# Kernel optimization log

Measured on AMD Instinct MI355X. Metric: run time of the kernel, lower is better.

## Reference

```python
import jax, jax.numpy as jnp
import numpy as np

N_NODES = 1024
BATCH = 64
N = N_NODES * BATCH          # 65536 total nodes
BBX, LBL = 7, 1
H1, H2, H3 = 512, 16, 4096
LAT = 512
NCLS = 160
N_EDGES = 262144


def setup_inputs() -> dict:
    key = jax.random.key(0)
    ks = jax.random.split(key, 20)
    g = lambda k, shape: (jax.random.normal(k, shape, jnp.float32) * 0.02)
    inp = dict(
        E=jax.random.randint(ks[0], (2, N_EDGES), 0, N, dtype=jnp.int64),
        X_data=jax.random.normal(ks[1], (N, BBX + LBL), jnp.float32),
        class_labels=jax.random.uniform(ks[2], (BATCH * NCLS,), jnp.float32),
        # GCNConv weights (no bias, no normalize, no self-loops)
        W_g1=g(ks[3], (BBX + LBL, H1)),
        W_g2=g(ks[4], (H1, H2)),
        # dense layers ([in, out] convention; y = x @ W + b)
        W_box=g(ks[5], (BBX, H2)), b_box=jnp.zeros((H2,), jnp.float32),
        W_lbl=g(ks[6], (LBL, H2)), b_lbl=jnp.zeros((H2,), jnp.float32),
        W_d1=g(ks[7], (H2 * N_NODES, H3)), b_d1=jnp.zeros((H3,), jnp.float32),
        W_d2=g(ks[8], (H2 * N_NODES + NCLS, H3)), b_d2=jnp.zeros((H3,), jnp.float32),
        W_d3=g(ks[9], (H3, H3)), b_d3=jnp.zeros((H3,), jnp.float32),
        W_z=g(ks[10], (H3, LAT)), b_z=jnp.zeros((LAT,), jnp.float32),
    )
    return inp


def reference(E, X_data, class_labels, W_g1, W_g2, W_box, b_box, W_lbl, b_lbl,
              W_d1, b_d1, W_d2, b_d2, W_d3, b_d3, W_z, b_z):
    relu = jax.nn.relu
    src, dst = E[0], E[1]
    # GCNConv (normalize=False, add_self_loops=False, bias=False):
    # out[i] = sum_{(j->i) in E} (x @ W)[j]
    x = jax.ops.segment_sum((X_data @ W_g1)[src], dst, num_segments=N)   # [N, H1]
    x = jax.ops.segment_sum((x @ W_g2)[src], dst, num_segments=N)        # [N, H2]
    x = x.reshape(BATCH, N_NODES * H2)                                   # [B, 16*num_nodes]
    boxes = relu(X_data[:, 1:].reshape(BATCH, N_NODES, BBX) @ W_box + b_box)
    labels = relu(X_data[:, :1].reshape(BATCH, N_NODES, LBL) @ W_lbl + b_lbl)
    mix = (boxes + labels).reshape(BATCH, N_NODES * H2)
    mix = relu(mix @ W_d1 + b_d1)                                        # [B, H3]
    cls = class_labels.reshape(BATCH, NCLS)
    x = jnp.concatenate([cls, x], axis=-1)                               # [B, NCLS + 16*num_nodes]
    x = relu(x @ W_d2 + b_d2)
    x = x + mix
    x = relu(x @ W_d3 + b_d3)
    x = relu(x @ W_d3 + b_d3)
    z_mean = relu(x @ W_z + b_z)
    z_logvar = relu(x @ W_z + b_z)
    return (z_mean, z_logvar)
```

## Files before the change

kernel.cpp:

```cpp
#include <hip/hip_runtime.h>
#include <stdint.h>

typedef unsigned short u16;
typedef short bf16x8 __attribute__((ext_vector_type(8)));
typedef short bf16x4 __attribute__((ext_vector_type(4)));
typedef float f32x4 __attribute__((ext_vector_type(4)));

#define NTOT   65536
#define NB     64
#define NEDGE  262144
#define H3     4096
#define LATD   512
#define NCLS_  160
#define K1     16384
#define K2     16544

static __device__ __forceinline__ u16 f2b(float f) {
  uint32_t x = __float_as_uint(f);
  return (u16)((x + 0x7FFFu + ((x >> 16) & 1u)) >> 16);
}

__global__ void k_hist(const int* __restrict__ E, int* __restrict__ cnt,
                       const float* __restrict__ Wg1, const float* __restrict__ Wg2,
                       float* __restrict__ Wc) {
  int e = blockIdx.x * 256 + threadIdx.x;
  atomicAdd(&cnt[E[NEDGE + e]], 1);
  if (blockIdx.x == 0 && threadIdx.x < 128) {
    int c = threadIdx.x >> 4, h = threadIdx.x & 15;
    float acc = 0.f;
    for (int k = 0; k < 512; ++k) acc += Wg1[c * 512 + k] * Wg2[k * 16 + h];
    Wc[c * 16 + h] = acc;
  }
}

__global__ __launch_bounds__(1024) void k_scan(const int* __restrict__ cnt,
                                               int* __restrict__ off,
                                               int* __restrict__ cur) {
  __shared__ int wsum[16];
  const int t = threadIdx.x;
  const int lane = t & 63, w = t >> 6;
  const int base = t << 6;
  int s = 0;
  const int4* c4 = (const int4*)(cnt + base);
  #pragma unroll 4
  for (int i = 0; i < 16; ++i) { int4 v = c4[i]; s += v.x + v.y + v.z + v.w; }
  int sc = s;
  #pragma unroll
  for (int d = 1; d < 64; d <<= 1) {
    int u = __shfl_up(sc, d);
    if (lane >= d) sc += u;
  }
  if (lane == 63) wsum[w] = sc;
  __syncthreads();
  if (w == 0 && lane < 16) {
    int v = wsum[lane];
    #pragma unroll
    for (int d = 1; d < 16; d <<= 1) {
      int u = __shfl_up(v, d);
      if (lane >= d) v += u;
    }
    wsum[lane] = v;
  }
  __syncthreads();
  int run = (w == 0 ? 0 : wsum[w - 1]) + (sc - s);
  int4* o4 = (int4*)(off + base);
  int4* u4 = (int4*)(cur + base);
  #pragma unroll 4
  for (int i = 0; i < 16; ++i) {
    int4 v = c4[i];
    int4 r;
    r.x = run; run += v.x;
    r.y = run; run += v.y;
    r.z = run; run += v.z;
    r.w = run; run += v.w;
    o4[i] = r; u4[i] = r;
  }
}

__global__ void k_scatter(const int* __restrict__ E, int* __restrict__ cur,
                          int* __restrict__ csr) {
  int e = blockIdx.x * 256 + threadIdx.x;
  int p = atomicAdd(&cur[E[NEDGE + e]], 1);
  csr[p] = E[e];
}

__global__ void k_gather(const int* __restrict__ off, const int* __restrict__ cnt,
                         const int* __restrict__ csr, const float* __restrict__ In,
                         float* __restrict__ Out) {
  int t = blockIdx.x * 256 + threadIdx.x;
  int n = t >> 3, c = t & 7;
  int b = off[n], e = b + cnt[n];
  float acc = 0.f;
  for (int j = b; j < e; ++j) acc += In[(size_t)csr[j] * 8 + c];
  Out[(size_t)n * 8 + c] = acc;
}

__global__ void k_nodes(const float* __restrict__ S2, const float* __restrict__ Wc,
                        const float* __restrict__ X,
                        const float* __restrict__ Wbox, const float* __restrict__ bbox,
                        const float* __restrict__ Wlbl, const float* __restrict__ blbl,
                        const float* __restrict__ cls,
                        u16* __restrict__ Abuf, u16* __restrict__ Mbuf) {
  int idx = blockIdx.x * 256 + threadIdx.x;
  if (idx < NB * NCLS_) {
    int m = idx / NCLS_, i = idx - m * NCLS_;
    Abuf[(size_t)m * K2 + i] = f2b(cls[idx]);
  }
  if (idx >= NTOT * 16) return;
  int n = idx >> 4, h = idx & 15;
  int m = n >> 10, nl = n & 1023;
  const float* s2 = S2 + (size_t)n * 8;
  float xg = 0.f;
  #pragma unroll
  for (int c = 0; c < 8; ++c) xg += s2[c] * Wc[c * 16 + h];
  Abuf[(size_t)m * K2 + 160 + nl * 16 + h] = f2b(xg);
  const float* xr = X + (size_t)n * 8;
  float box = bbox[h];
  #pragma unroll
  for (int c = 0; c < 7; ++c) box += xr[1 + c] * Wbox[c * 16 + h];
  box = box > 0.f ? box : 0.f;
  float lb = xr[0] * Wlbl[h] + blbl[h];
  lb = lb > 0.f ? lb : 0.f;
  Mbuf[(size_t)m * K1 + nl * 16 + h] = f2b(box + lb);
}

__device__ __forceinline__ void gl16(const void* g, void* l) {
  __builtin_amdgcn_global_load_lds(
      (const __attribute__((address_space(1))) unsigned int*)g,
      (__attribute__((address_space(3))) unsigned int*)l, 16, 0, 0);
}

#define GEMM_STEP(ST, ArD, WrD, AwR, WwR)                                      \
  {                                                                            \
    const int i1 = (ST) + 1 < ns ? (ST) + 1 : ns - 1;                          \
    const int i2 = (ST) + 2 < ns ? (ST) + 2 : ns - 1;                          \
    gl16(gA + (size_t)i1 * 32, &AwR[t * 8]);                                   \
    __builtin_amdgcn_sched_barrier(0);                                         \
    bf16x8 a  = *(const bf16x8*)(&ArD[aoff]);                                  \
    bf16x8 b0 = *(const bf16x8*)(&WrD[fo]);                                    \
    bf16x8 b1 = *(const bf16x8*)(&WrD[fo + 512]);                              \
    bf16x8 b2 = *(const bf16x8*)(&WrD[fo + 1024]);                             \
    bf16x8 b3 = *(const bf16x8*)(&WrD[fo + 1536]);                             \
    bf16x4 p0 = { (short)f2b(wr0.x), (short)f2b(wr1.x),                        \
                  (short)f2b(wr2.x), (short)f2b(wr3.x) };                      \
    bf16x4 p1 = { (short)f2b(wr0.y), (short)f2b(wr1.y),                        \
                  (short)f2b(wr2.y), (short)f2b(wr3.y) };                      \
    *(bf16x4*)(&WwR[wtOff0]) = p0;                                             \
    *(bf16x4*)(&WwR[wtOff1]) = p1;                                             \
    const float* gWn = gW + (size_t)i2 * stepW;                                \
    wr0 = *(const float2*)(gWn);                                               \
    wr1 = *(const float2*)(gWn + Nw);                                          \
    wr2 = *(const float2*)(gWn + 2 * Nw);                                      \
    wr3 = *(const float2*)(gWn + 3 * Nw);                                      \
    ac0 = __builtin_amdgcn_mfma_f32_16x16x32_bf16(a, b0, ac0, 0, 0, 0);        \
    ac1 = __builtin_amdgcn_mfma_f32_16x16x32_bf16(a, b1, ac1, 0, 0, 0);        \
    ac2 = __builtin_amdgcn_mfma_f32_16x16x32_bf16(a, b2, ac2, 0, 0, 0);        \
    ac3 = __builtin_amdgcn_mfma_f32_16x16x32_bf16(a, b3, ac3, 0, 0, 0);        \
    asm volatile("s_waitcnt lgkmcnt(0)" ::: "memory");                         \
    asm volatile("s_waitcnt vmcnt(4)" ::: "memory");                           \
    __builtin_amdgcn_s_barrier();                                              \
    asm volatile("" ::: "memory");                                             \
  }

__global__ __launch_bounds__(256) void k_gemm(
    const u16* __restrict__ A0, const u16* __restrict__ A1, int lda0, int lda1,
    const float* __restrict__ W0, const float* __restrict__ W1, int Nw,
    int tot0, int tot1, int per0, int per1, int slabBase1,
    float* __restrict__ Cs)
{
  __shared__ u16 lA0[2048];
  __shared__ u16 lA1[2048];
  __shared__ u16 lW0[2048];
  __shared__ u16 lW1[2048];

  const u16* A; int lda; const float* W; int tot, per, slab;
  if (blockIdx.z == 0) { A = A0; lda = lda0; W = W0; tot = tot0; per = per0; slab = blockIdx.y; }
  else                 { A = A1; lda = lda1; W = W1; tot = tot1; per = per1; slab = slabBase1 + blockIdx.y; }

  const int n0  = blockIdx.x << 6;
  const int sp0 = blockIdx.y * per;
  int ns = tot - sp0; if (ns > per) ns = per;
  if (ns <= 0) return;
  const int t  = threadIdx.x;
  const int l  = t & 63;
  const int wv = t >> 6;

  const int rA  = t >> 2;
  const int cAg = (t & 3) ^ ((rA >> 1) & 3);
  const u16* gA = A + (size_t)rA * lda + cAg * 8 + (size_t)sp0 * 32;

  const int q  = t >> 5;
  const int nc = (t & 31) * 2;
  const int mW = (t & 31) & 3;
  const float* gW = W + (size_t)(sp0 * 32 + 4 * q) * Nw + n0 + nc;
  const int wtOff0 = nc * 32 + ((4 * q) ^ (8 * mW));
  const int wtOff1 = wtOff0 + 32;
  const size_t stepW = (size_t)32 * Nw;

  const int rAf  = (wv << 4) + (l & 15);
  const int aoff = rAf * 32 + (((l >> 4) ^ ((rAf >> 1) & 3)) << 3);
  const int g4 = l >> 4;
  const int li = l & 15;
  const int mR = (li >> 1) & 3;
  const int fo = li * 32 + 8 * (g4 ^ mR);

  f32x4 ac0 = {0.f, 0.f, 0.f, 0.f}, ac1 = ac0, ac2 = ac0, ac3 = ac0;

  float2 wr0, wr1, wr2, wr3;
  gl16(gA, &lA0[t * 8]);
  __builtin_amdgcn_sched_barrier(0);
  wr0 = *(const float2*)(gW);
  wr1 = *(const float2*)(gW + Nw);
  wr2 = *(const float2*)(gW + 2 * Nw);
  wr3 = *(const float2*)(gW + 3 * Nw);
  {
    bf16x4 p0 = { (short)f2b(wr0.x), (short)f2b(wr1.x),
                  (short)f2b(wr2.x), (short)f2b(wr3.x) };
    bf16x4 p1 = { (short)f2b(wr0.y), (short)f2b(wr1.y),
                  (short)f2b(wr2.y), (short)f2b(wr3.y) };
    *(bf16x4*)(&lW0[wtOff0]) = p0;
    *(bf16x4*)(&lW0[wtOff1]) = p1;
    const int i1p = 1 < ns ? 1 : 0;
    const float* gWn = gW + (size_t)i1p * stepW;
    wr0 = *(const float2*)(gWn);
    wr1 = *(const float2*)(gWn + Nw);
    wr2 = *(const float2*)(gWn + 2 * Nw);
    wr3 = *(const float2*)(gWn + 3 * Nw);
  }
  asm volatile("s_waitcnt lgkmcnt(0)" ::: "memory");
  asm volatile("s_waitcnt vmcnt(4)" ::: "memory");
  __builtin_amdgcn_s_barrier();
  asm volatile("" ::: "memory");

  int st = 0;
  for (; st + 2 <= ns; st += 2) {
    GEMM_STEP(st,     lA0, lW0, lA1, lW1);
    GEMM_STEP(st + 1, lA1, lW1, lA0, lW0);
  }
  if (st < ns) {
    GEMM_STEP(st, lA0, lW0, lA1, lW1);
  }

  const int col  = n0 + li;
  const int row0 = (wv << 4) + (g4 << 2);
  float* base = Cs + (size_t)slab * NB * Nw;
  #pragma unroll
  for (int j = 0; j < 4; ++j) {
    float* cp = base + (size_t)(row0 + j) * Nw + col;
    cp[0]  = ac0[j];
    cp[16] = ac1[j];
    cp[32] = ac2[j];
    cp[48] = ac3[j];
  }
}

__global__ void k_ep12(const float* __restrict__ Cs,
                       const float* __restrict__ b1, const float* __restrict__ b2,
                       u16* __restrict__ A3) {
  int i = blockIdx.x * 256 + threadIdx.x;
  if (i >= NB * H3) return;
  float mix = b1[i & (H3 - 1)];
  float v   = b2[i & (H3 - 1)];
  #pragma unroll 4
  for (int s = 0; s < 16; ++s)  mix += Cs[(size_t)s * (NB * H3) + i];
  #pragma unroll 4
  for (int s = 16; s < 32; ++s) v   += Cs[(size_t)s * (NB * H3) + i];
  mix = mix > 0.f ? mix : 0.f;
  v   = v   > 0.f ? v   : 0.f;
  A3[i] = f2b(v + mix);
}

__global__ void k_ep(const float* __restrict__ Cs, int nslab, int slabElems,
                     const float* __restrict__ bias, u16* __restrict__ outb,
                     int colmask, int total) {
  int i = blockIdx.x * 256 + threadIdx.x;
  if (i >= total) return;
  float v = bias[i & colmask];
  #pragma unroll 4
  for (int s = 0; s < nslab; ++s) v += Cs[(size_t)s * slabElems + i];
  v = v > 0.f ? v : 0.f;
  outb[i] = f2b(v);
}

__global__ void k_ep5(const float* __restrict__ Cs, int nslab,
                      const float* __restrict__ bz, float* __restrict__ out) {
  int i = blockIdx.x * 256 + threadIdx.x;
  if (i >= NB * LATD) return;
  float v = bz[i & 511];
  #pragma unroll 4
  for (int s = 0; s < nslab; ++s) v += Cs[(size_t)s * (NB * LATD) + i];
  v = v > 0.f ? v : 0.f;
  out[i] = v;
  out[NB * LATD + i] = v;
}

extern "C" void kernel_launch(void* const* d_in, const int* in_sizes, int n_in,
                              void* d_out, int out_size, void* d_ws, size_t ws_size,
                              hipStream_t stream) {
  const int*   E    = (const int*)d_in[0];
  const float* X    = (const float*)d_in[1];
  const float* cls  = (const float*)d_in[2];
  const float* Wg1  = (const float*)d_in[3];
  const float* Wg2  = (const float*)d_in[4];
  const float* Wbox = (const float*)d_in[5];
  const float* bbox = (const float*)d_in[6];
  const float* Wlbl = (const float*)d_in[7];
  const float* blbl = (const float*)d_in[8];
  const float* Wd1  = (const float*)d_in[9];
  const float* bd1  = (const float*)d_in[10];
  const float* Wd2  = (const float*)d_in[11];
  const float* bd2  = (const float*)d_in[12];
  const float* Wd3  = (const float*)d_in[13];
  const float* bd3  = (const float*)d_in[14];
  const float* Wz   = (const float*)d_in[15];
  const float* bz   = (const float*)d_in[16];

  char* ws = (char*)d_ws;
  int*   cnt  = (int*)  (ws + 0x000000);
  int*   off  = (int*)  (ws + 0x040000);
  int*   cur  = (int*)  (ws + 0x080000);
  int*   csr  = (int*)  (ws + 0x0C0000);
  float* S1   = (float*)(ws + 0x1C0000);
  float* S2   = (float*)(ws + 0x3C0000);
  float* Wc   = (float*)(ws + 0x5C0000);
  u16*   A3   = (u16*)  (ws + 0x5C1000);
  u16*   A4   = (u16*)  (ws + 0x641000);
  u16*   A5   = (u16*)  (ws + 0x6C1000);
  u16*   Mbuf = (u16*)  (ws + 0x741000);
  u16*   Abuf = (u16*)  (ws + 0x941000);
  float* Cslb = (float*)(ws + 0xB50000);

  hipMemsetAsync(cnt, 0, 0x40000, stream);
  k_hist   <<<NEDGE / 256, 256, 0, stream>>>(E, cnt, Wg1, Wg2, Wc);
  k_scan   <<<1, 1024, 0, stream>>>(cnt, off, cur);
  k_scatter<<<NEDGE / 256, 256, 0, stream>>>(E, cur, csr);
  k_gather <<<NTOT * 8 / 256, 256, 0, stream>>>(off, cnt, csr, X,  S1);
  k_gather <<<NTOT * 8 / 256, 256, 0, stream>>>(off, cnt, csr, S1, S2);
  k_nodes  <<<NTOT * 16 / 256, 256, 0, stream>>>(S2, Wc, X, Wbox, bbox, Wlbl, blbl,
                                                 cls, Abuf, Mbuf);

  { dim3 g(64, 16, 2);
    k_gemm<<<g, 256, 0, stream>>>(Mbuf, Abuf, K1, K2, Wd1, Wd2, H3,
                                  512, 517, 32, 33, 16, Cslb); }
  k_ep12<<<NB * H3 / 256, 256, 0, stream>>>(Cslb, bd1, bd2, A3);

  { dim3 g(64, 16, 1);
    k_gemm<<<g, 256, 0, stream>>>(A3, A3, H3, H3, Wd3, Wd3, H3,
                                  128, 128, 8, 8, 0, Cslb); }
  k_ep<<<NB * H3 / 256, 256, 0, stream>>>(Cslb, 16, NB * H3, bd3, A4, H3 - 1, NB * H3);

  { dim3 g(64, 16, 1);
    k_gemm<<<g, 256, 0, stream>>>(A4, A4, H3, H3, Wd3, Wd3, H3,
                                  128, 128, 8, 8, 0, Cslb); }
  k_ep<<<NB * H3 / 256, 256, 0, stream>>>(Cslb, 16, NB * H3, bd3, A5, H3 - 1, NB * H3);

  { dim3 g(8, 32, 1);
    k_gemm<<<g, 256, 0, stream>>>(A5, A5, H3, H3, Wz, Wz, LATD,
                                  128, 128, 4, 4, 0, Cslb); }
  k_ep5<<<NB * LATD / 256, 256, 0, stream>>>(Cslb, 32, bz, (float*)d_out);
}
```

Before: 309.0 us.

## Register-stage A and W loads two steps ahead, use packed bf16 convert

Replaces the direct global-to-LDS load of the A tile with an ordinary vector load into registers that is written to LDS later. A and W tiles are now prefetched into two rotating register sets, three steps ahead of use, instead of one step. The explicit vmcnt wait is removed, and the software rounding to bf16 becomes the hardware v_cvt_pk_bf16_f32 instruction. The goal is deeper latency hiding in this memory-bound GEMM, at the cost of more registers and an extra LDS write for A.

```diff
diff --git a/kernel.cpp b/kernel.cpp
--- a/kernel.cpp
+++ b/kernel.cpp
@@ -124,40 +124,40 @@
   Mbuf[(size_t)m * K1 + nl * 16 + h] = f2b(box + lb);
 }
 
-__device__ __forceinline__ void gl16(const void* g, void* l) {
-  __builtin_amdgcn_global_load_lds(
-      (const __attribute__((address_space(1))) unsigned int*)g,
-      (__attribute__((address_space(3))) unsigned int*)l, 16, 0, 0);
-}
-
-#define GEMM_STEP(ST, ArD, WrD, AwR, WwR)                                      \
+#define CVTPK(dst, lo, hi) \
+  asm("v_cvt_pk_bf16_f32 %0, %1, %2" : "=v"(dst) : "v"(lo), "v"(hi))
+
+#define GEMM_STEP(ST, ArD, WrD, AwR, WwR, aS, w0S, w1S, w2S, w3S)              \
   {                                                                            \
-    const int i1 = (ST) + 1 < ns ? (ST) + 1 : ns - 1;                          \
-    const int i2 = (ST) + 2 < ns ? (ST) + 2 : ns - 1;                          \
-    gl16(gA + (size_t)i1 * 32, &AwR[t * 8]);                                   \
-    __builtin_amdgcn_sched_barrier(0);                                         \
     bf16x8 a  = *(const bf16x8*)(&ArD[aoff]);                                  \
     bf16x8 b0 = *(const bf16x8*)(&WrD[fo]);                                    \
     bf16x8 b1 = *(const bf16x8*)(&WrD[fo + 512]);                              \
     bf16x8 b2 = *(const bf16x8*)(&WrD[fo + 1024]);                             \
     bf16x8 b3 = *(const bf16x8*)(&WrD[fo + 1536]);                             \
-    bf16x4 p0 = { (short)f2b(wr0.x), (short)f2b(wr1.x),                        \
-                  (short)f2b(wr2.x), (short)f2b(wr3.x) };                      \
-    bf16x4 p1 = { (short)f2b(wr0.y), (short)f2b(wr1.y),                        \
-                  (short)f2b(wr2.y), (short)f2b(wr3.y) };                      \
-    *(bf16x4*)(&WwR[wtOff0]) = p0;                                             \
-    *(bf16x4*)(&WwR[wtOff1]) = p1;                                             \
-    const float* gWn = gW + (size_t)i2 * stepW;                                \
-    wr0 = *(const float2*)(gWn);                                               \
-    wr1 = *(const float2*)(gWn + Nw);                                          \
-    wr2 = *(const float2*)(gWn + 2 * Nw);                                      \
-    wr3 = *(const float2*)(gWn + 3 * Nw);                                      \
+                \
+    *(int4*)(&AwR[t * 8]) = aS;                                                \
+    uint32_t r0, r1, r2, r3;                                                   \
+    CVTPK(r0, w0S.x, w1S.x);                                                   \
+    CVTPK(r1, w2S.x, w3S.x);                                                   \
+    CVTPK(r2, w0S.y, w1S.y);                                                   \
+    CVTPK(r3, w2S.y, w3S.y);                                                   \
+    { uint2 p0 = {r0, r1}; uint2 p1 = {r2, r3};                                \
+      *(uint2*)(&WwR[wtOff0]) = p0;                                            \
+      *(uint2*)(&WwR[wtOff1]) = p1; }                                          \
+                        \
+    { const int ii = (ST) + 3 < ns ? (ST) + 3 : ns - 1;                        \
+      const u16*  ga = gA + (size_t)ii * 32;                                   \
+      const float* gw = gW + (size_t)ii * stepW;                               \
+      aS  = *(const int4*)ga;                                                  \
+      w0S = *(const float2*)(gw);                                              \
+      w1S = *(const float2*)(gw + Nw);                                         \
+      w2S = *(const float2*)(gw + 2 * Nw);                                     \
+      w3S = *(const float2*)(gw + 3 * Nw); }                                   \
     ac0 = __builtin_amdgcn_mfma_f32_16x16x32_bf16(a, b0, ac0, 0, 0, 0);        \
     ac1 = __builtin_amdgcn_mfma_f32_16x16x32_bf16(a, b1, ac1, 0, 0, 0);        \
     ac2 = __builtin_amdgcn_mfma_f32_16x16x32_bf16(a, b2, ac2, 0, 0, 0);        \
     ac3 = __builtin_amdgcn_mfma_f32_16x16x32_bf16(a, b3, ac3, 0, 0, 0);        \
     asm volatile("s_waitcnt lgkmcnt(0)" ::: "memory");                         \
-    asm volatile("s_waitcnt vmcnt(4)" ::: "memory");                           \
     __builtin_amdgcn_s_barrier();                                              \
     asm volatile("" ::: "memory");                                             \
   }
@@ -206,39 +206,57 @@
 
   f32x4 ac0 = {0.f, 0.f, 0.f, 0.f}, ac1 = ac0, ac2 = ac0, ac3 = ac0;
 
-  float2 wr0, wr1, wr2, wr3;
-  gl16(gA, &lA0[t * 8]);
-  __builtin_amdgcn_sched_barrier(0);
-  wr0 = *(const float2*)(gW);
-  wr1 = *(const float2*)(gW + Nw);
-  wr2 = *(const float2*)(gW + 2 * Nw);
-  wr3 = *(const float2*)(gW + 3 * Nw);
+  int4 aS0, aS1;
+  float2 w00, w01, w02, w03;
+  float2 w10, w11, w12, w13;
+
+  const int i1 = 1 < ns ? 1 : ns - 1;
+  const int i2 = 2 < ns ? 2 : ns - 1;
+  aS0 = *(const int4*)(gA);
+  w00 = *(const float2*)(gW);
+  w01 = *(const float2*)(gW + Nw);
+  w02 = *(const float2*)(gW + 2 * Nw);
+  w03 = *(const float2*)(gW + 3 * Nw);
   {
-    bf16x4 p0 = { (short)f2b(wr0.x), (short)f2b(wr1.x),
-                  (short)f2b(wr2.x), (short)f2b(wr3.x) };
-    bf16x4 p1 = { (short)f2b(wr0.y), (short)f2b(wr1.y),
-                  (short)f2b(wr2.y), (short)f2b(wr3.y) };
-    *(bf16x4*)(&lW0[wtOff0]) = p0;
-    *(bf16x4*)(&lW0[wtOff1]) = p1;
-    const int i1p = 1 < ns ? 1 : 0;
-    const float* gWn = gW + (size_t)i1p * stepW;
-    wr0 = *(const float2*)(gWn);
-    wr1 = *(const float2*)(gWn + Nw);
-    wr2 = *(const float2*)(gWn + 2 * Nw);
-    wr3 = *(const float2*)(gWn + 3 * Nw);
+    const u16*  ga = gA + (size_t)i1 * 32;
+    const float* gw = gW + (size_t)i1 * stepW;
+    aS1 = *(const int4*)ga;
+    w10 = *(const float2*)(gw);
+    w11 = *(const float2*)(gw + Nw);
+    w12 = *(const float2*)(gw + 2 * Nw);
+    w13 = *(const float2*)(gw + 3 * Nw);
+  }
+  *(int4*)(&lA0[t * 8]) = aS0;
+  {
+    uint32_t r0, r1, r2, r3;
+    CVTPK(r0, w00.x, w01.x);
+    CVTPK(r1, w02.x, w03.x);
+    CVTPK(r2, w00.y, w01.y);
+    CVTPK(r3, w02.y, w03.y);
+    uint2 p0 = {r0, r1}; uint2 p1 = {r2, r3};
+    *(uint2*)(&lW0[wtOff0]) = p0;
+    *(uint2*)(&lW0[wtOff1]) = p1;
+  }
+  {
+    const u16*  ga = gA + (size_t)i2 * 32;
+    const float* gw = gW + (size_t)i2 * stepW;
+    aS0 = *(const int4*)ga;
+    w00 = *(const float2*)(gw);
+    w01 = *(const float2*)(gw + Nw);
+    w02 = *(const float2*)(gw + 2 * Nw);
+    w03 = *(const float2*)(gw + 3 * Nw);
   }
   asm volatile("s_waitcnt lgkmcnt(0)" ::: "memory");
-  asm volatile("s_waitcnt vmcnt(4)" ::: "memory");
   __builtin_amdgcn_s_barrier();
   asm volatile("" ::: "memory");
 
   int st = 0;
   for (; st + 2 <= ns; st += 2) {
-    GEMM_STEP(st,     lA0, lW0, lA1, lW1);
-    GEMM_STEP(st + 1, lA1, lW1, lA0, lW0);
+    GEMM_STEP(st,     lA0, lW0, lA1, lW1, aS1, w10, w11, w12, w13);
+    GEMM_STEP(st + 1, lA1, lW1, lA0, lW0, aS0, w00, w01, w02, w03);
   }
   if (st < ns) {
-    GEMM_STEP(st, lA0, lW0, lA1, lW1);
+    GEMM_STEP(st, lA0, lW0, lA1, lW1, aS1, w10, w11, w12, w13);
   }
 
   const int col  = n0 + li;
```

Measured after the change: 306.7 us. Within noise of the previous version (-0.8%).
